# Kernel optimization log

Measured on AMD Instinct MI355X. Metric: run time of the kernel, lower is better.

Reference implementation:

```python
import jax, jax.numpy as jnp
import numpy as np

N = 8192       # node_num
F_IN = 256     # src_feature
F_OUT = 128    # out_feature
NEG_SLOPE = 0.2  # standard GAT leakyrelu slope
MASK_VAL = -1e12


def setup_inputs() -> dict:
    key = jax.random.key(0)
    k1, k2, k3, k4, k5, k6 = jax.random.split(key, 6)
    x = jax.random.normal(k1, (N, F_IN), dtype=jnp.float32)
    adj = jax.random.randint(k2, (N, N), 0, 2, dtype=jnp.int32)  # 0/1 adjacency mask
    # xavier-uniform-like scales
    W = jax.random.normal(k3, (F_IN, F_OUT), dtype=jnp.float32) * np.float32(1.0 / np.sqrt(F_IN))
    a1 = jax.random.normal(k4, (F_OUT,), dtype=jnp.float32) * np.float32(0.1)  # att[:F_OUT]
    a2 = jax.random.normal(k5, (F_OUT,), dtype=jnp.float32) * np.float32(0.1)  # att[F_OUT:]
    bias = jax.random.normal(k6, (F_OUT,), dtype=jnp.float32) * np.float32(0.1)
    return {"x": x, "adj": adj, "W": W, "a1": a1, "a2": a2, "bias": bias}


def reference(x, adj, W, a1, a2, bias):
    # h = x @ W1  (src_h == dst_h for int src_dst_feature)
    h = x @ W  # [N, F_OUT]
    # e[i,j] = leakyrelu(att^T [h_i || h_j]) decomposed as (h@a1)_i + (h@a2)_j
    s_src = h @ a1  # [N]
    s_dst = h @ a2  # [N]
    e = jax.nn.leaky_relu(s_src[:, None] + s_dst[None, :], NEG_SLOPE)  # [N, N]
    masked = jnp.where(adj > 0, e, jnp.float32(MASK_VAL))
    attention = jax.nn.softmax(masked, axis=1)  # [N, N]
    # dropout in eval mode = identity; aggregate neighbor features
    out = attention @ h + bias  # [N, F_OUT]
    return out
```

## Files before the change

### kernel.cpp

```cpp
#include <hip/hip_runtime.h>
#include <cstdint>
#include <cstddef>

#define NN 8192
#define FIN 256
#define FOUT 128
#define SLOPE 0.2f
#define SHIFT 8.0f

typedef float f32x4 __attribute__((ext_vector_type(4)));
typedef __bf16 bf16x8 __attribute__((ext_vector_type(8)));
typedef int i32x4 __attribute__((ext_vector_type(4)));
typedef unsigned int u32x4 __attribute__((ext_vector_type(4)));

__device__ __forceinline__ unsigned short f2bf(float f) {
  return __builtin_bit_cast(unsigned short, (__bf16)f);
}

__device__ __forceinline__ void async_cp16(void* lds, const void* g) {
  __builtin_amdgcn_global_load_lds(
      (const __attribute__((address_space(1))) void*)g,
      (__attribute__((address_space(3))) void*)lds, 16, 0, 0);
}

__global__ __launch_bounds__(256) void k_pack(const int* __restrict__ adj,
                                              unsigned int* __restrict__ adjp2) {
  const int gw = (blockIdx.x * 256 + threadIdx.x) >> 6;
  const int lane = threadIdx.x & 63;
  #pragma unroll 1
  for (int qt = gw; qt < 8192 * 32; qt += 8192) {
    const int row = qt >> 5;
    const int j256 = qt & 31;
    const int* p = adj + (size_t)row * NN + j256 * 256 + lane;
    const int a0 = p[0];
    const int a1 = p[64];
    const int a2 = p[128];
    const int a3 = p[192];
    const unsigned long long m0 = __ballot(a0 != 0);
    const unsigned long long m1 = __ballot(a1 != 0);
    const unsigned long long m2 = __ballot(a2 != 0);
    const unsigned long long m3 = __ballot(a3 != 0);
    if (lane < 8) {
      const int wg = j256 * 8 + lane;
      const int CB = wg >> 5, ch = (wg >> 1) & 15, w = wg & 1;
      const int RB = row >> 7, r = row & 127;
      const int sel = lane >> 1;
      const unsigned long long mk =
          (sel == 0) ? m0 : (sel == 1) ? m1 : (sel == 2) ? m2 : m3;
      const unsigned int val = (lane & 1) ? (unsigned)(mk >> 32) : (unsigned)mk;
      adjp2[(((size_t)RB * 8 + CB) * 16 + ch) * 256 + w * 128 + r] = val;
    }
  }
}

__global__ __launch_bounds__(256, 4) void k_hw(const float* __restrict__ x,
                                               const float* __restrict__ W,
                                               const float* __restrict__ a1,
                                               const float* __restrict__ a2,
                                               unsigned short* __restrict__ ht,
                                               float* __restrict__ Etab,
                                               unsigned short* __restrict__ FbfF,
                                               unsigned short* __restrict__ FbfF2) {
  __shared__ float xs[8][256];
  __shared__ unsigned short tile[128][8];
  const int tid = threadIdx.x;
  const int rowbase = blockIdx.x * 8;

  #pragma unroll
  for (int it = 0; it < 2; ++it) {
    int fi = it * 1024 + tid * 4;
    int r = fi >> 8, k = fi & 255;
    *(f32x4*)&xs[r][k] = *(const f32x4*)(x + (size_t)(rowbase + r) * FIN + k);
  }
  __syncthreads();

  const int r = tid >> 5;
  const int cg = tid & 31;
  f32x4 acc = {0.f, 0.f, 0.f, 0.f};

  #pragma unroll 8
  for (int k = 0; k < FIN; ++k) {
    f32x4 wv = *(const f32x4*)(W + k * FOUT + cg * 4);
    float xv = xs[r][k];
    acc[0] += xv * wv[0];
    acc[1] += xv * wv[1];
    acc[2] += xv * wv[2];
    acc[3] += xv * wv[3];
  }

  #pragma unroll
  for (int c = 0; c < 4; ++c) tile[cg * 4 + c][r] = f2bf(acc[c]);

  f32x4 av1 = *(const f32x4*)(a1 + cg * 4);
  f32x4 av2 = *(const f32x4*)(a2 + cg * 4);
  float s1 = acc[0] * av1[0] + acc[1] * av1[1] + acc[2] * av1[2] + acc[3] * av1[3];
  float s2 = acc[0] * av2[0] + acc[1] * av2[1] + acc[2] * av2[2] + acc[3] * av2[3];
  #pragma unroll
  for (int off = 16; off > 0; off >>= 1) {
    s1 += __shfl_xor(s1, off, 64);
    s2 += __shfl_xor(s2, off, 64);
  }
  if (cg == 0) {
    const int row = rowbase + r;
    float c0 = s1 + SHIFT;
    float c = fmaxf(c0, SLOPE * c0);
    Etab[(size_t)row * 2]     = __expf(s1 - c);
    Etab[(size_t)row * 2 + 1] = __expf(SLOPE * s1 - c);
    FbfF[row]  = f2bf(__expf(s2));
    FbfF2[row] = f2bf(__expf(SLOPE * s2));
  }
  __syncthreads();

  if (tid < 128) {
    u32x4 v = *(const u32x4*)&tile[tid][0];
    *(u32x4*)(ht + (size_t)tid * NN + rowbase) = v;
  }
}

__global__ __launch_bounds__(512, 4) void k_gat(const unsigned int* __restrict__ adjp2,
                                                const unsigned short* __restrict__ ht,
                                                const float* __restrict__ Etab,
                                                const unsigned short* __restrict__ FbfF,
                                                const unsigned short* __restrict__ FbfF2,
                                                float* __restrict__ part,
                                                float* __restrict__ denp) {
  __shared__ unsigned short sH[2][128 * 64];
  __shared__ unsigned int sAp[16][2][128];
  __shared__ unsigned short sF[2][128];

  const int tid = threadIdx.x;
  const int wave = tid >> 6;
  const int lane = tid & 63;
  const int quad = lane >> 4;
  const int m = lane & 15;
  const int rowbase = (int)(blockIdx.x >> 3) * 128;
  const int colbase = (int)(blockIdx.x & 7) * 1024;
  const int CB = (int)(blockIdx.x & 7);
  const int row = rowbase + wave * 16 + m;

  bf16x8 pm, pinv, pones;
  #pragma unroll
  for (int jj = 0; jj < 8; ++jj) {
    pm[jj] = (__bf16)(float)m;
    pinv[jj] = (__bf16)0.03125f;
    pones[jj] = (__bf16)1.0f;
  }
  f32x4 z = {0.f, 0.f, 0.f, 0.f};
  f32x4 rp = __builtin_amdgcn_mfma_f32_16x16x32_bf16(pm, pinv, z, 0, 0, 0);
  f32x4 cp = __builtin_amdgcn_mfma_f32_16x16x32_bf16(pinv, pm, z, 0, 0, 0);
  int rowmap[4], colmap[4];
  #pragma unroll
  for (int r = 0; r < 4; ++r) {
    rowmap[r] = ((int)(rp[r] + 0.5f)) & 15;
    colmap[r] = ((int)(cp[r] + 0.5f)) & 15;
  }

  const float E  = Etab[(size_t)row * 2];
  const float E2 = Etab[(size_t)row * 2 + 1];

  f32x4 acc[8];
  #pragma unroll
  for (int t = 0; t < 8; ++t) acc[t] = z;
  f32x4 den = z;

  const unsigned short* srcH[2];
  #pragma unroll
  for (int il = 0; il < 2; ++il) {
    const int i = wave * 2 + il;
    const int f = i * 8 + (lane >> 3);
    const int g = (lane & 7) ^ (lane >> 3);
    srcH[il] = ht + (size_t)f * NN + colbase + g * 8;
  }
  const unsigned short* srcF = nullptr;
  if (wave == 1) {
    srcF = (lane < 8) ? (FbfF + colbase + lane * 8)
                      : (FbfF2 + colbase + (lane - 8) * 8);
  }

  auto stage = [&](int b, int c) {
    #pragma unroll
    for (int il = 0; il < 2; ++il)
      async_cp16(&sH[b][(wave * 2 + il) * 512], srcH[il] + c * 64);
    if (wave == 1 && lane < 16) async_cp16(&sF[b][0], srcF + c * 64);
  };

  auto compute = [&](int cs, int c) {
    #pragma unroll
    for (int k32 = 0; k32 < 2; ++k32) {
      const unsigned int word = sAp[c][k32][wave * 16 + m];
      const unsigned int byt = (word >> (quad * 8)) & 0xffu;
      const int jl = k32 * 32 + quad * 8;
      u32x4 Fq = *(const u32x4*)&sF[cs][jl];
      u32x4 Gq = *(const u32x4*)&sF[cs][64 + jl];

      bf16x8 af;
      #pragma unroll
      for (int p = 0; p < 4; ++p) {
        const unsigned fp = Fq[p], gp = Gq[p];
        const float Flo = __builtin_bit_cast(float, fp << 16);
        const float Fhi = __builtin_bit_cast(float, fp & 0xffff0000u);
        const float Glo = __builtin_bit_cast(float, gp << 16);
        const float Ghi = __builtin_bit_cast(float, gp & 0xffff0000u);
        const float wlo = fmaxf(E * Flo, E2 * Glo);
        const float whi = fmaxf(E * Fhi, E2 * Ghi);
        af[p * 2]     = (byt & (1u << (p * 2)))     ? (__bf16)wlo : (__bf16)0.0f;
        af[p * 2 + 1] = (byt & (1u << (p * 2 + 1))) ? (__bf16)whi : (__bf16)0.0f;
      }

      const int s0 = (k32 * 4 + quad) ^ (m & 7);
      #pragma unroll
      for (int t = 0; t < 8; ++t) {
        bf16x8 bt = __builtin_bit_cast(bf16x8,
            *(const u32x4*)&sH[cs][(t * 16 + m) * 64 + s0 * 8]);
        acc[t] = __builtin_amdgcn_mfma_f32_16x16x32_bf16(af, bt, acc[t], 0, 0, 0);
      }
      den = __builtin_amdgcn_mfma_f32_16x16x32_bf16(af, pones, den, 0, 0, 0);
    }
  };

  {
    const unsigned int* srcAp = adjp2 + (size_t)blockIdx.x * 4096;
    #pragma unroll
    for (int il = 0; il < 2; ++il)
      async_cp16(((unsigned int*)sAp) + (wave * 2 + il) * 256,
                 srcAp + (wave * 2 + il) * 256 + lane * 4);
  }
  stage(0, 0);

  #pragma unroll 1
  for (int c = 0; c < 16; c += 2) {
    __syncthreads();
    stage(1, c + 1);
    compute(0, c);
    __syncthreads();
    if (c + 2 < 16) stage(0, c + 2);
    compute(1, c + 1);
  }

  float* sOut = (float*)&sH[0][0];
  #pragma unroll
  for (int h = 0; h < 2; ++h) {
    __syncthreads();
    #pragma unroll
    for (int r = 0; r < 4; ++r) {
      #pragma unroll
      for (int tt = 0; tt < 4; ++tt) {
        sOut[(wave * 16 + rowmap[r]) * 64 + tt * 16 + colmap[r]] =
            acc[h * 4 + tt][r];
      }
    }
    __syncthreads();
    #pragma unroll
    for (int i = 0; i < 4; ++i) {
      const int v = i * 512 + tid;
      const int rl = v >> 4, c4 = v & 15;
      *(f32x4*)&part[((size_t)CB * NN + rowbase + rl) * FOUT + h * 64 + c4 * 4] =
          ((const f32x4*)sOut)[v];
    }
  }
  if (m == 0) {
    #pragma unroll
    for (int r = 0; r < 4; ++r)
      denp[(size_t)CB * NN + rowbase + wave * 16 + rowmap[r]] = den[r];
  }
}

__global__ __launch_bounds__(256) void k_fin(const float* __restrict__ part,
                                             const float* __restrict__ denp,
                                             const float* __restrict__ bias,
                                             float* __restrict__ out) {
  const int i4 = blockIdx.x * 256 + threadIdx.x;
  const int rowi = i4 >> 5;
  const int f = (i4 & 31) * 4;
  float den = 0.f;
  f32x4 s = {0.f, 0.f, 0.f, 0.f};
  #pragma unroll
  for (int cb = 0; cb < 8; ++cb) {
    den += denp[(size_t)cb * NN + rowi];
    f32x4 p = *(const f32x4*)&part[((size_t)cb * NN + rowi) * FOUT + f];
    s[0] += p[0]; s[1] += p[1]; s[2] += p[2]; s[3] += p[3];
  }
  const float inv = 1.0f / den;
  f32x4 b = *(const f32x4*)(bias + f);
  f32x4 v = {s[0] * inv + b[0], s[1] * inv + b[1],
             s[2] * inv + b[2], s[3] * inv + b[3]};
  *(f32x4*)(out + (size_t)rowi * FOUT + f) = v;
}

extern "C" void kernel_launch(void* const* d_in, const int* in_sizes, int n_in,
                              void* d_out, int out_size, void* d_ws, size_t ws_size,
                              hipStream_t stream) {
  const float* x    = (const float*)d_in[0];
  const int*   adj  = (const int*)d_in[1];
  const float* W    = (const float*)d_in[2];
  const float* a1   = (const float*)d_in[3];
  const float* a2   = (const float*)d_in[4];
  const float* bias = (const float*)d_in[5];
  float* out = (float*)d_out;

  char* ws = (char*)d_ws;
  unsigned short* ht = (unsigned short*)ws;
  float* Etab = (float*)(ws + (size_t)2 * 1024 * 1024);
  unsigned short* FbfF =
      (unsigned short*)(ws + (size_t)2 * 1024 * 1024 + 64 * 1024);
  unsigned short* FbfF2 = FbfF + NN;
  unsigned int* adjp2 =
      (unsigned int*)(ws + (size_t)2 * 1024 * 1024 + 128 * 1024);
  float* part = (float*)(ws + (size_t)12 * 1024 * 1024);
  float* denp = (float*)(ws + (size_t)44 * 1024 * 1024);

  k_pack<<<2048, 256, 0, stream>>>(adj, adjp2);
  k_hw<<<NN / 8, 256, 0, stream>>>(x, W, a1, a2, ht, Etab, FbfF, FbfF2);
  k_gat<<<512, 512, 0, stream>>>(adjp2, ht, Etab, FbfF, FbfF2, part, denp);
  k_fin<<<(NN * FOUT / 4) / 256, 256, 0, stream>>>(part, denp, bias, out);
}
```

Baseline: 442.1 us.

## Fuse adjacency bit-packing into attention kernel with register-prefetched ballot packing

Removes the separate packing kernel and has the attention kernel read the int32 adjacency directly. Each wave loads 16 rows by 64 columns into registers one chunk ahead and packs them with ballots into a double-buffered LDS bitmask. The main loop changes from two chunks per iteration to one chunk with a ping-pong buffer. This drops a kernel launch and the write and read-back of the packed mask, but raises per-block global loads and register pressure inside the compute loop.

```diff
diff --git a/kernel.cpp b/kernel.cpp
--- a/kernel.cpp
+++ b/kernel.cpp
@@ -21,36 +21,6 @@
   __builtin_amdgcn_global_load_lds(
       (const __attribute__((address_space(1))) void*)g,
       (__attribute__((address_space(3))) void*)lds, 16, 0, 0);
-}
-
-__global__ __launch_bounds__(256) void k_pack(const int* __restrict__ adj,
-                                              unsigned int* __restrict__ adjp2) {
-  const int gw = (blockIdx.x * 256 + threadIdx.x) >> 6;
-  const int lane = threadIdx.x & 63;
-  #pragma unroll 1
-  for (int qt = gw; qt < 8192 * 32; qt += 8192) {
-    const int row = qt >> 5;
-    const int j256 = qt & 31;
-    const int* p = adj + (size_t)row * NN + j256 * 256 + lane;
-    const int a0 = p[0];
-    const int a1 = p[64];
-    const int a2 = p[128];
-    const int a3 = p[192];
-    const unsigned long long m0 = __ballot(a0 != 0);
-    const unsigned long long m1 = __ballot(a1 != 0);
-    const unsigned long long m2 = __ballot(a2 != 0);
-    const unsigned long long m3 = __ballot(a3 != 0);
-    if (lane < 8) {
-      const int wg = j256 * 8 + lane;
-      const int CB = wg >> 5, ch = (wg >> 1) & 15, w = wg & 1;
-      const int RB = row >> 7, r = row & 127;
-      const int sel = lane >> 1;
-      const unsigned long long mk =
-          (sel == 0) ? m0 : (sel == 1) ? m1 : (sel == 2) ? m2 : m3;
-      const unsigned int val = (lane & 1) ? (unsigned)(mk >> 32) : (unsigned)mk;
-      adjp2[(((size_t)RB * 8 + CB) * 16 + ch) * 256 + w * 128 + r] = val;
-    }
-  }
 }
 
 __global__ __launch_bounds__(256, 4) void k_hw(const float* __restrict__ x,
@@ -117,7 +87,7 @@
   }
 }
 
-__global__ __launch_bounds__(512, 4) void k_gat(const unsigned int* __restrict__ adjp2,
+__global__ __launch_bounds__(512, 4) void k_gat(const int* __restrict__ adj,
                                                 const unsigned short* __restrict__ ht,
                                                 const float* __restrict__ Etab,
                                                 const unsigned short* __restrict__ FbfF,
@@ -125,7 +95,7 @@
                                                 float* __restrict__ part,
                                                 float* __restrict__ denp) {
   __shared__ unsigned short sH[2][128 * 64];
-  __shared__ unsigned int sAp[16][2][128];
+  __shared__ unsigned int sAp[2][128][2];
   __shared__ unsigned short sF[2][128];
 
   const int tid = threadIdx.x;
@@ -163,6 +133,22 @@
   for (int t = 0; t < 8; ++t) acc[t] = z;
   f32x4 den = z;
 
+  const int* adjRow = adj + (size_t)(rowbase + wave * 16) * NN + colbase + lane;
+  int aregs[16];
+  auto loadA = [&](int c) {
+    #pragma unroll
+    for (int r = 0; r < 16; ++r)
+      aregs[r] = adjRow[(size_t)r * NN + c * 64];
+  };
+  auto packA = [&](int b) {
+    #pragma unroll
+    for (int r = 0; r < 16; ++r) {
+      const unsigned long long mk = __ballot(aregs[r] != 0);
+      if (lane == 0)
+        *(unsigned long long*)&sAp[b][wave * 16 + r][0] = mk;
+    }
+  };
+
   const unsigned short* srcH[2];
   #pragma unroll
   for (int il = 0; il < 2; ++il) {
@@ -184,10 +170,10 @@
     if (wave == 1 && lane < 16) async_cp16(&sF[b][0], srcF + c * 64);
   };
 
-  auto compute = [&](int cs, int c) {
+  auto compute = [&](int cs) {
     #pragma unroll
     for (int k32 = 0; k32 < 2; ++k32) {
-      const unsigned int word = sAp[c][k32][wave * 16 + m];
+      const unsigned int word = sAp[cs][wave * 16 + m][k32];
       const unsigned int byt = (word >> (quad * 8)) & 0xffu;
       const int jl = k32 * 32 + quad * 8;
       u32x4 Fq = *(const u32x4*)&sF[cs][jl];
@@ -218,23 +204,21 @@
     }
   };
 
-  {
-    const unsigned int* srcAp = adjp2 + (size_t)blockIdx.x * 4096;
-    #pragma unroll
-    for (int il = 0; il < 2; ++il)
-      async_cp16(((unsigned int*)sAp) + (wave * 2 + il) * 256,
-                 srcAp + (wave * 2 + il) * 256 + lane * 4);
-  }
+  loadA(0);
+  packA(0);
+  loadA(1);
   stage(0, 0);
 
   #pragma unroll 1
-  for (int c = 0; c < 16; c += 2) {
+  for (int c = 0; c < 16; ++c) {
+    const int cs = c & 1, ns = cs ^ 1;
     __syncthreads();
-    stage(1, c + 1);
-    compute(0, c);
-    __syncthreads();
-    if (c + 2 < 16) stage(0, c + 2);
-    compute(1, c + 1);
+    if (c + 1 < 16) {
+      packA(ns);
+      loadA(c + 2 < 16 ? c + 2 : 15);
+      stage(ns, c + 1);
+    }
+    compute(cs);
   }
 
   float* sOut = (float*)&sH[0][0];
@@ -304,13 +288,10 @@
   unsigned short* FbfF =
       (unsigned short*)(ws + (size_t)2 * 1024 * 1024 + 64 * 1024);
   unsigned short* FbfF2 = FbfF + NN;
-  unsigned int* adjp2 =
-      (unsigned int*)(ws + (size_t)2 * 1024 * 1024 + 128 * 1024);
-  float* part = (float*)(ws + (size_t)12 * 1024 * 1024);
-  float* denp = (float*)(ws + (size_t)44 * 1024 * 1024);
-
-  k_pack<<<2048, 256, 0, stream>>>(adj, adjp2);
+  float* part = (float*)(ws + (size_t)4 * 1024 * 1024);
+  float* denp = (float*)(ws + (size_t)36 * 1024 * 1024);
+
   k_hw<<<NN / 8, 256, 0, stream>>>(x, W, a1, a2, ht, Etab, FbfF, FbfF2);
-  k_gat<<<512, 512, 0, stream>>>(adjp2, ht, Etab, FbfF, FbfF2, part, denp);
+  k_gat<<<512, 512, 0, stream>>>(adj, ht, Etab, FbfF, FbfF2, part, denp);
   k_fin<<<(NN * FOUT / 4) / 256, 256, 0, stream>>>(part, denp, bias, out);
 }
```

Measured after the change: 443.2 us. Within noise of the previous version (+0.3%).
